# Kernel tuning notes

Measured on AMD Instinct MI355X. Metric: run time of the kernel, lower is better.

Reference implementation:

```python
import jax, jax.numpy as jnp
import numpy as np

D_MODEL = 1024
NUM_HEADS = 16
DEPTH = D_MODEL // NUM_HEADS
MAX_LEN = 5000


def _make_pe(d_model=D_MODEL, max_len=MAX_LEN):
    # Faithful to torch PositionalEncoding: pe shape [max_len, 1, d_model]
    position = np.arange(max_len, dtype=np.float32)[:, None]
    div_term = np.exp(np.arange(0, d_model, 2, dtype=np.float32) * (-np.log(10000.0) / d_model))
    pe = np.zeros((max_len, d_model), dtype=np.float32)
    pe[:, 0::2] = np.sin(position * div_term)
    pe[:, 1::2] = np.cos(position * div_term)
    return jnp.asarray(pe[:, None, :])  # [max_len, 1, d_model]


def setup_inputs() -> dict:
    key = jax.random.key(0)
    ks = jax.random.split(key, 11)
    B, S, D = 4, 2048, D_MODEL
    s = 1.0 / np.sqrt(D)
    inp = {
        "v": jax.random.normal(ks[0], (B, S, D), jnp.float32),
        "k": jax.random.normal(ks[1], (B, S, D), jnp.float32),
        "q": jax.random.normal(ks[2], (B, S, D), jnp.float32),
        "wq_w": jax.random.normal(ks[3], (D, D), jnp.float32) * s,
        "wq_b": jnp.zeros((D,), jnp.float32),
        "wk_w": jax.random.normal(ks[4], (D, D), jnp.float32) * s,
        "wk_b": jnp.zeros((D,), jnp.float32),
        "wv_w": jax.random.normal(ks[5], (D, D), jnp.float32) * s,
        "wv_b": jnp.zeros((D,), jnp.float32),
        "dense_w": jax.random.normal(ks[6], (D, D), jnp.float32) * s,
        "dense_b": jnp.zeros((D,), jnp.float32),
        "pe": _make_pe(),
    }
    return inp


def _split_heads(x, B):
    # [B, S, D] -> [B, H, S, depth]
    return x.reshape(B, -1, NUM_HEADS, DEPTH).transpose(0, 2, 1, 3)


def reference(v, k, q, wq_w, wq_b, wk_w, wk_b, wv_w, wv_b, dense_w, dense_b, pe):
    B = q.shape[0]
    # Faithful bug-reproduction: pe[:batch] has shape [B, 1, D], broadcast over seq.
    pe_b = pe[:B]  # [B, 1, D]
    q = q + pe_b
    k = k + pe_b
    v = v + pe_b
    # Linear layers (torch: x @ W.T + b)
    qh = _split_heads(q @ wq_w.T + wq_b, B)  # [B,H,Sq,d]
    kh = _split_heads(k @ wk_w.T + wk_b, B)  # [B,H,Sk,d]
    vh = _split_heads(v @ wv_w.T + wv_b, B)  # [B,H,Sk,d]
    scale = 1.0 / jnp.sqrt(jnp.float32(DEPTH))
    logits = jnp.einsum("bhqd,bhkd->bhqk", qh, kh) * scale
    attn = jax.nn.softmax(logits, axis=-1)
    out = jnp.einsum("bhqk,bhkd->bhqd", attn, vh)
    out = out.transpose(0, 2, 1, 3).reshape(B, -1, D_MODEL)
    return out @ dense_w.T + dense_b
```

## Files before the change

kernel.cpp:

```cpp
#include <hip/hip_runtime.h>
#include <hip/hip_bf16.h>

typedef short short8 __attribute__((ext_vector_type(8)));
typedef float f32x4 __attribute__((ext_vector_type(4)));
typedef float f32x16 __attribute__((ext_vector_type(16)));
typedef unsigned int uint4v __attribute__((ext_vector_type(4)));

#define MFMA16(a, b, c) __builtin_amdgcn_mfma_f32_16x16x32_bf16(a, b, c, 0, 0, 0)
#define MFMA32(a, b, c) __builtin_amdgcn_mfma_f32_32x32x16_bf16(a, b, c, 0, 0, 0)

typedef __attribute__((address_space(1))) const unsigned int gas_u32;
typedef __attribute__((address_space(3))) unsigned int las_u32;

__device__ inline void gll16(const void* g, void* l) {
    __builtin_amdgcn_global_load_lds((gas_u32*)g, (las_u32*)l, 16, 0, 0);
}

__device__ inline unsigned short f2bf(float f) {
    unsigned u = __builtin_bit_cast(unsigned, f);
    u += 0x7fff + ((u >> 16) & 1);
    return (unsigned short)(u >> 16);
}

__device__ inline unsigned pk_trunc(float a, float b) {
    unsigned ua = __builtin_bit_cast(unsigned, a);
    unsigned ub = __builtin_bit_cast(unsigned, b);
    return (ua >> 16) | (ub & 0xFFFF0000u);
}

__device__ inline float exp2_fast(float x) {
#if __has_builtin(__builtin_amdgcn_exp2f)
    return __builtin_amdgcn_exp2f(x);
#else
    float r; asm("v_exp_f32 %0, %1" : "=v"(r) : "v"(x)); return r;
#endif
}

__device__ inline void pl32_swap(unsigned &a, unsigned &b) {
    asm volatile("v_permlane32_swap_b32 %0, %1" : "+v"(a), "+v"(b));
}

__global__ void pe_cast3(const float* __restrict__ q, const float* __restrict__ k,
                         const float* __restrict__ v, const float* __restrict__ pe,
                         unsigned short* __restrict__ oq, unsigned short* __restrict__ ok,
                         unsigned short* __restrict__ ov) {
    const float* x = (blockIdx.y == 0) ? q : (blockIdx.y == 1) ? k : v;
    unsigned short* o = (blockIdx.y == 0) ? oq : (blockIdx.y == 1) ? ok : ov;
    int i = blockIdx.x * 256 + threadIdx.x;
    long e = (long)i * 4;
    int b = (int)(e >> 21);
    int d = (int)(e & 1023);
    float4 xv = reinterpret_cast<const float4*>(x)[i];
    float4 pv = *reinterpret_cast<const float4*>(pe + b * 1024 + d);
    ushort4 r;
    r.x = f2bf(xv.x + pv.x); r.y = f2bf(xv.y + pv.y);
    r.z = f2bf(xv.z + pv.z); r.w = f2bf(xv.w + pv.w);
    reinterpret_cast<ushort4*>(o)[i] = r;
}

__global__ void wcast4(const float* __restrict__ w0, const float* __restrict__ w1,
                       const float* __restrict__ w2, const float* __restrict__ w3,
                       unsigned short* __restrict__ o0) {
    const float* w = (blockIdx.y == 0) ? w0 : (blockIdx.y == 1) ? w1
                   : (blockIdx.y == 2) ? w2 : w3;
    unsigned short* o = o0 + (size_t)blockIdx.y * 1024 * 1024;
    int i = blockIdx.x * 256 + threadIdx.x;
    float4 xv = reinterpret_cast<const float4*>(w)[i];
    ushort4 r;
    r.x = f2bf(xv.x); r.y = f2bf(xv.y); r.z = f2bf(xv.z); r.w = f2bf(xv.w);
    reinterpret_cast<ushort4*>(o)[i] = r;
}

template <int MODE>
__global__ __launch_bounds__(256) void gemm_bt(const unsigned short* __restrict__ A,
                                               const unsigned short* __restrict__ W,
                                               const float* __restrict__ bias,
                                               void* __restrict__ out, float scale) {
    const int K = 1024;
    __shared__ unsigned short lsA[128 * 32];
    __shared__ unsigned short lsB[128 * 32];
    int tid = threadIdx.x;
    int wave = tid >> 6, lane = tid & 63, lg = lane >> 4, l15 = lane & 15;
    int brow = blockIdx.x * 128;
    int bcol = blockIdx.y * 128;
    int wr = wave >> 1, wc = wave & 1;

    f32x4 zero4 = {0.f, 0.f, 0.f, 0.f};
    f32x4 acc[4][4];
#pragma unroll
    for (int m = 0; m < 4; ++m)
#pragma unroll
        for (int n = 0; n < 4; ++n) acc[m][n] = zero4;

    for (int k0 = 0; k0 < K; k0 += 32) {
#pragma unroll
        for (int j = 0; j < 2; ++j) {
            int c = j * 256 + wave * 64 + lane;
            const unsigned short* srcA = A + ((long)(brow + (c >> 2)) * K + k0 + (c & 3) * 8);
            const unsigned short* srcB = W + ((long)(bcol + (c >> 2)) * K + k0 + (c & 3) * 8);
            char* dstA = (char*)lsA + (j * 256 + wave * 64) * 16;
            char* dstB = (char*)lsB + (j * 256 + wave * 64) * 16;
            gll16(srcA, dstA);
            gll16(srcB, dstB);
        }
        __syncthreads();
        short8 af[4], bf_[4];
#pragma unroll
        for (int m = 0; m < 4; ++m) {
            int row = wr * 64 + m * 16 + l15;
            af[m] = *(const short8*)((const char*)lsA + row * 64 + lg * 16);
        }
#pragma unroll
        for (int n = 0; n < 4; ++n) {
            int col = wc * 64 + n * 16 + l15;
            bf_[n] = *(const short8*)((const char*)lsB + col * 64 + lg * 16);
        }
#pragma unroll
        for (int m = 0; m < 4; ++m)
#pragma unroll
            for (int n = 0; n < 4; ++n) acc[m][n] = MFMA16(af[m], bf_[n], acc[m][n]);
        __syncthreads();
    }

#pragma unroll
    for (int m = 0; m < 4; ++m)
#pragma unroll
        for (int n = 0; n < 4; ++n) {
            int col = bcol + wc * 64 + n * 16 + l15;
            float bv = bias[col];
#pragma unroll
            for (int r = 0; r < 4; ++r) {
                int row = brow + wr * 64 + m * 16 + lg * 4 + r;
                float v = (acc[m][n][r] + bv) * scale;
                if (MODE == 0) {
                    int b = row >> 11, s = row & 2047, h = col >> 6, d = col & 63;
                    ((unsigned short*)out)[(((long)(b * 16 + h) * 2048 + s) * 64 + d)] = f2bf(v);
                } else if (MODE == 1) {
                    ((float*)out)[(long)row * 1024 + col] = v;
                } else {
                    int b = row >> 11, s = row & 2047;
                    ((unsigned short*)out)[((long)(b * 1024 + col)) * 2048 + s] = f2bf(v);
                }
            }
        }
}

__global__ __launch_bounds__(256) void attn_kernel(const unsigned short* __restrict__ Qh,
                                                   const unsigned short* __restrict__ Kh,
                                                   const unsigned short* __restrict__ Vt,
                                                   unsigned short* __restrict__ Om) {
    const int S = 2048;
    int flat = blockIdx.x;
    int nf_ = (flat & 7) * 128 + (flat >> 3);
    int qt = nf_ & 15;
    int bh = nf_ >> 4;
    int b = bh >> 4, h = bh & 15;

    int tid = threadIdx.x, wave = tid >> 6, lane = tid & 63;
    int l31 = lane & 31, hi = lane >> 5;

    __shared__ __align__(16) unsigned short Kl[2][4096];
    __shared__ __align__(16) unsigned short Vtl[2][4096];

    const unsigned short* Qb = Qh + (long)bh * S * 64;
    const unsigned short* Kb = Kh + (long)bh * S * 64;
    const unsigned short* Vb = Vt + (long)bh * 64 * S;

    int colS = ((((tid & 7) * 16) ^ (((tid >> 3) & 7) << 4)) >> 1);
    const unsigned short* srcK = Kb + (tid >> 3) * 64 + colS;
    const unsigned short* srcV = Vb + (tid >> 3) * 2048 + colS;

    short8 aq[4];
    {
        const unsigned short* qrow = Qb + (long)(qt * 128 + wave * 32 + l31) * 64 + hi * 8;
#pragma unroll
        for (int s = 0; s < 4; ++s) aq[s] = *(const short8*)(qrow + s * 16);
    }

    f32x16 oacc[2], lacc;
#pragma unroll
    for (int r = 0; r < 16; ++r) { oacc[0][r] = 0.f; oacc[1][r] = 0.f; lacc[r] = 0.f; }

    const short8 ones8 = {0x3F80, 0x3F80, 0x3F80, 0x3F80, 0x3F80, 0x3F80, 0x3F80, 0x3F80};

    int rb0 = l31 * 128;
    int swz = (l31 & 7) << 4;

#define STAGE(kt, bi) do {                                              \
        const unsigned short* sk = srcK + (kt) * 4096;                  \
        gll16(sk,         (char*)Kl[bi] + wave * 1024);                 \
        gll16(sk + 2048,  (char*)Kl[bi] + 4096 + wave * 1024);          \
        const unsigned short* sv = srcV + (kt) * 64;                    \
        gll16(sv,         (char*)Vtl[bi] + wave * 1024);                \
        gll16(sv + 65536, (char*)Vtl[bi] + 4096 + wave * 1024);         \
    } while (0)

    STAGE(0, 0);
    __syncthreads();

    for (int kt = 0; kt < S / 64; ++kt) {
        int cur = kt & 1;
        if (kt < S / 64 - 1) STAGE(kt + 1, cur ^ 1);

        const char* KlC = (const char*)Kl[cur];
        const char* VlC = (const char*)Vtl[cur];

        f32x16 sacc[2];
#pragma unroll
        for (int r = 0; r < 16; ++r) { sacc[0][r] = 0.f; sacc[1][r] = 0.f; }
#pragma unroll
        for (int blk = 0; blk < 2; ++blk)
#pragma unroll
            for (int s = 0; s < 4; ++s) {
                short8 kf = *(const short8*)(KlC + blk * 4096 + rb0 + ((32 * s + 16 * hi) ^ swz));
                sacc[blk] = MFMA32(kf, aq[s], sacc[blk]);
            }

#pragma unroll
        for (int blk = 0; blk < 2; ++blk)
#pragma unroll
            for (int r = 0; r < 16; ++r) sacc[blk][r] = exp2_fast(sacc[blk][r]);

#pragma unroll
        for (int s = 0; s < 4; ++s) {
            const int blk = s >> 1, base = (s & 1) * 8;
            unsigned q0 = pk_trunc(sacc[blk][base + 0], sacc[blk][base + 1]);
            unsigned q1 = pk_trunc(sacc[blk][base + 2], sacc[blk][base + 3]);
            unsigned q2 = pk_trunc(sacc[blk][base + 4], sacc[blk][base + 5]);
            unsigned q3 = pk_trunc(sacc[blk][base + 6], sacc[blk][base + 7]);
            pl32_swap(q0, q2);
            pl32_swap(q1, q3);
            uint4v pw; pw[0] = q0; pw[1] = q1; pw[2] = q2; pw[3] = q3;
            short8 pa = __builtin_bit_cast(short8, pw);
#pragma unroll
            for (int dblk = 0; dblk < 2; ++dblk) {
                short8 vf = *(const short8*)(VlC + dblk * 4096 + rb0 + ((32 * s + 16 * hi) ^ swz));
                oacc[dblk] = MFMA32(pa, vf, oacc[dblk]);
            }
            lacc = MFMA32(pa, ones8, lacc);
        }
        __syncthreads();
    }
#undef STAGE

    float inv[16];
#pragma unroll
    for (int r = 0; r < 16; ++r) inv[r] = 1.0f / lacc[r];

    int qrow0 = qt * 128 + wave * 32 + 4 * hi;
#pragma unroll
    for (int dblk = 0; dblk < 2; ++dblk)
#pragma unroll
        for (int r = 0; r < 16; ++r) {
            int qrow = qrow0 + (r & 3) + 8 * (r >> 2);
            int d = h * 64 + dblk * 32 + l31;
            float v = oacc[dblk][r] * inv[r];
            Om[((long)b * 2048 + qt * 0 + qrow) * 1024 + d] = f2bf(v);
        }
}

extern "C" void kernel_launch(void* const* d_in, const int* in_sizes, int n_in,
                              void* d_out, int out_size, void* d_ws, size_t ws_size,
                              hipStream_t stream) {
    const float* v_in = (const float*)d_in[0];
    const float* k_in = (const float*)d_in[1];
    const float* q_in = (const float*)d_in[2];
    const float* wq_w = (const float*)d_in[3];
    const float* wq_b = (const float*)d_in[4];
    const float* wk_w = (const float*)d_in[5];
    const float* wk_b = (const float*)d_in[6];
    const float* wv_w = (const float*)d_in[7];
    const float* wv_b = (const float*)d_in[8];
    const float* wd_w = (const float*)d_in[9];
    const float* wd_b = (const float*)d_in[10];
    const float* pe   = (const float*)d_in[11];

    const long SZ = 8192L * 1024 * 2;
    char* ws = (char*)d_ws;
    unsigned short* xq = (unsigned short*)(ws + 0);
    unsigned short* xk = (unsigned short*)(ws + SZ);
    unsigned short* xv = (unsigned short*)(ws + 2 * SZ);
    unsigned short* qh = (unsigned short*)(ws + 3 * SZ);
    unsigned short* kh = (unsigned short*)(ws + 4 * SZ);
    unsigned short* vt = (unsigned short*)(ws + 5 * SZ);
    unsigned short* wqb16 = (unsigned short*)(ws + 6 * SZ);
    unsigned short* wkb16 = wqb16 + 1024 * 1024;
    unsigned short* wvb16 = wkb16 + 1024 * 1024;
    unsigned short* wdb16 = wvb16 + 1024 * 1024;

    pe_cast3<<<dim3(8192, 3), 256, 0, stream>>>(q_in, k_in, v_in, pe, xq, xk, xv);
    wcast4<<<dim3(1024, 4), 256, 0, stream>>>(wq_w, wk_w, wv_w, wd_w, wqb16);

    const float QSCALE = 0.125f * 1.44269504088896f;
    dim3 gg(64, 8);
    gemm_bt<0><<<gg, 256, 0, stream>>>(xq, wqb16, wq_b, qh, QSCALE);
    gemm_bt<0><<<gg, 256, 0, stream>>>(xk, wkb16, wk_b, kh, 1.0f);
    gemm_bt<2><<<gg, 256, 0, stream>>>(xv, wvb16, wv_b, vt, 1.0f);
    unsigned short* om = xq;
    attn_kernel<<<1024, 256, 0, stream>>>(qh, kh, vt, om);
    gemm_bt<1><<<gg, 256, 0, stream>>>(om, wdb16, wd_b, d_out, 1.0f);
}
```

Measured before the change: 230.6 us.

## Merge QKV GEMMs into one launch and triple-buffer attention K/V loads

Replaces the three separate Q/K/V projection launches with a single 3D-grid launch whose z index selects input, weight, bias and output layout. The dense GEMM becomes its own specialised kernel. The attention kernel moves from double to triple buffering of the K/V tiles: it prefetches two tiles ahead, waits with explicit vmcnt counts and a raw barrier, and drops the trailing syncthreads. The goal is to cut launch gaps and tail effects and to hide more global-load latency, at the cost of more LDS per block and fragile hand-written wait counts.

Result: no change. 233.9 us (+1.4%).

```diff
diff --git a/kernel.cpp b/kernel.cpp
--- a/kernel.cpp
+++ b/kernel.cpp
@@ -71,11 +71,93 @@
     reinterpret_cast<ushort4*>(o)[i] = r;
 }
 
-template <int MODE>
-__global__ __launch_bounds__(256) void gemm_bt(const unsigned short* __restrict__ A,
-                                               const unsigned short* __restrict__ W,
-                                               const float* __restrict__ bias,
-                                               void* __restrict__ out, float scale) {
+__global__ __launch_bounds__(256) void gemm_qkv(const unsigned short* __restrict__ X0,
+                                                const unsigned short* __restrict__ W0,
+                                                const float* __restrict__ bq,
+                                                const float* __restrict__ bk,
+                                                const float* __restrict__ bv,
+                                                unsigned short* __restrict__ oq,
+                                                unsigned short* __restrict__ ok,
+                                                unsigned short* __restrict__ ov,
+                                                float qscale) {
+    const int K = 1024;
+    int z = blockIdx.z;
+    const unsigned short* A = X0 + (size_t)z * 8192 * 1024;
+    const unsigned short* W = W0 + (size_t)z * 1024 * 1024;
+    const float* bias = (z == 0) ? bq : (z == 1) ? bk : bv;
+    unsigned short* out = (z == 0) ? oq : (z == 1) ? ok : ov;
+    float scale = (z == 0) ? qscale : 1.0f;
+
+    __shared__ unsigned short lsA[128 * 32];
+    __shared__ unsigned short lsB[128 * 32];
+    int tid = threadIdx.x;
+    int wave = tid >> 6, lane = tid & 63, lg = lane >> 4, l15 = lane & 15;
+    int brow = blockIdx.x * 128;
+    int bcol = blockIdx.y * 128;
+    int wr = wave >> 1, wc = wave & 1;
+
+    f32x4 zero4 = {0.f, 0.f, 0.f, 0.f};
+    f32x4 acc[4][4];
+#pragma unroll
+    for (int m = 0; m < 4; ++m)
+#pragma unroll
+        for (int n = 0; n < 4; ++n) acc[m][n] = zero4;
+
+    for (int k0 = 0; k0 < K; k0 += 32) {
+#pragma unroll
+        for (int j = 0; j < 2; ++j) {
+            int c = j * 256 + wave * 64 + lane;
+            const unsigned short* srcA = A + ((long)(brow + (c >> 2)) * K + k0 + (c & 3) * 8);
+            const unsigned short* srcB = W + ((long)(bcol + (c >> 2)) * K + k0 + (c & 3) * 8);
+            char* dstA = (char*)lsA + (j * 256 + wave * 64) * 16;
+            char* dstB = (char*)lsB + (j * 256 + wave * 64) * 16;
+            gll16(srcA, dstA);
+            gll16(srcB, dstB);
+        }
+        __syncthreads();
+        short8 af[4], bf_[4];
+#pragma unroll
+        for (int m = 0; m < 4; ++m) {
+            int row = wr * 64 + m * 16 + l15;
+            af[m] = *(const short8*)((const char*)lsA + row * 64 + lg * 16);
+        }
+#pragma unroll
+        for (int n = 0; n < 4; ++n) {
+            int col = wc * 64 + n * 16 + l15;
+            bf_[n] = *(const short8*)((const char*)lsB + col * 64 + lg * 16);
+        }
+#pragma unroll
+        for (int m = 0; m < 4; ++m)
+#pragma unroll
+            for (int n = 0; n < 4; ++n) acc[m][n] = MFMA16(af[m], bf_[n], acc[m][n]);
+        __syncthreads();
+    }
+
+#pragma unroll
+    for (int m = 0; m < 4; ++m)
+#pragma unroll
+        for (int n = 0; n < 4; ++n) {
+            int col = bcol + wc * 64 + n * 16 + l15;
+            float bv_ = bias[col];
+#pragma unroll
+            for (int r = 0; r < 4; ++r) {
+                int row = brow + wr * 64 + m * 16 + lg * 4 + r;
+                float v = (acc[m][n][r] + bv_) * scale;
+                int b = row >> 11, s = row & 2047;
+                if (z < 2) {
+                    int h = col >> 6, d = col & 63;
+                    out[(((long)(b * 16 + h) * 2048 + s) * 64 + d)] = f2bf(v);
+                } else {
+                    out[((long)(b * 1024 + col)) * 2048 + s] = f2bf(v);
+                }
+            }
+        }
+}
+
+__global__ __launch_bounds__(256) void gemm_dense(const unsigned short* __restrict__ A,
+                                                  const unsigned short* __restrict__ W,
+                                                  const float* __restrict__ bias,
+                                                  float* __restrict__ out) {
     const int K = 1024;
     __shared__ unsigned short lsA[128 * 32];
     __shared__ unsigned short lsB[128 * 32];
@@ -131,16 +213,7 @@
 #pragma unroll
             for (int r = 0; r < 4; ++r) {
                 int row = brow + wr * 64 + m * 16 + lg * 4 + r;
-                float v = (acc[m][n][r] + bv) * scale;
-                if (MODE == 0) {
-                    int b = row >> 11, s = row & 2047, h = col >> 6, d = col & 63;
-                    ((unsigned short*)out)[(((long)(b * 16 + h) * 2048 + s) * 64 + d)] = f2bf(v);
-                } else if (MODE == 1) {
-                    ((float*)out)[(long)row * 1024 + col] = v;
-                } else {
-                    int b = row >> 11, s = row & 2047;
-                    ((unsigned short*)out)[((long)(b * 1024 + col)) * 2048 + s] = f2bf(v);
-                }
+                out[(long)row * 1024 + col] = acc[m][n][r] + bv;
             }
         }
 }
@@ -150,6 +223,7 @@
                                                    const unsigned short* __restrict__ Vt,
                                                    unsigned short* __restrict__ Om) {
     const int S = 2048;
+    const int NT = S / 64;
     int flat = blockIdx.x;
     int nf_ = (flat & 7) * 128 + (flat >> 3);
     int qt = nf_ & 15;
@@ -159,8 +233,8 @@
     int tid = threadIdx.x, wave = tid >> 6, lane = tid & 63;
     int l31 = lane & 31, hi = lane >> 5;
 
-    __shared__ __align__(16) unsigned short Kl[2][4096];
-    __shared__ __align__(16) unsigned short Vtl[2][4096];
+    __shared__ __align__(16) unsigned short Kl[3][4096];
+    __shared__ __align__(16) unsigned short Vtl[3][4096];
 
     const unsigned short* Qb = Qh + (long)bh * S * 64;
     const unsigned short* Kb = Kh + (long)bh * S * 64;
@@ -196,14 +270,17 @@
     } while (0)
 
     STAGE(0, 0);
-    __syncthreads();
-
-    for (int kt = 0; kt < S / 64; ++kt) {
-        int cur = kt & 1;
-        if (kt < S / 64 - 1) STAGE(kt + 1, cur ^ 1);
-
-        const char* KlC = (const char*)Kl[cur];
-        const char* VlC = (const char*)Vtl[cur];
+    STAGE(1, 1);
+
+    int bi = 0, sb = 2;
+    for (int kt = 0; kt < NT; ++kt) {
+        if (kt == NT - 1) { asm volatile("s_waitcnt vmcnt(0)" ::: "memory"); }
+        else              { asm volatile("s_waitcnt vmcnt(4)" ::: "memory"); }
+        __builtin_amdgcn_s_barrier();
+        if (kt < NT - 2) STAGE(kt + 2, sb);
+
+        const char* KlC = (const char*)Kl[bi];
+        const char* VlC = (const char*)Vtl[bi];
 
         f32x16 sacc[2];
 #pragma unroll
@@ -239,7 +316,8 @@
             }
             lacc = MFMA32(pa, ones8, lacc);
         }
-        __syncthreads();
+        bi = (bi == 2) ? 0 : bi + 1;
+        sb = (sb == 2) ? 0 : sb + 1;
     }
 #undef STAGE
 
@@ -255,7 +333,7 @@
             int qrow = qrow0 + (r & 3) + 8 * (r >> 2);
             int d = h * 64 + dblk * 32 + l31;
             float v = oacc[dblk][r] * inv[r];
-            Om[((long)b * 2048 + qt * 0 + qrow) * 1024 + d] = f2bf(v);
+            Om[((long)b * 2048 + qrow) * 1024 + d] = f2bf(v);
         }
 }
 
@@ -284,19 +362,15 @@
     unsigned short* kh = (unsigned short*)(ws + 4 * SZ);
     unsigned short* vt = (unsigned short*)(ws + 5 * SZ);
     unsigned short* wqb16 = (unsigned short*)(ws + 6 * SZ);
-    unsigned short* wkb16 = wqb16 + 1024 * 1024;
-    unsigned short* wvb16 = wkb16 + 1024 * 1024;
-    unsigned short* wdb16 = wvb16 + 1024 * 1024;
 
     pe_cast3<<<dim3(8192, 3), 256, 0, stream>>>(q_in, k_in, v_in, pe, xq, xk, xv);
     wcast4<<<dim3(1024, 4), 256, 0, stream>>>(wq_w, wk_w, wv_w, wd_w, wqb16);
 
     const float QSCALE = 0.125f * 1.44269504088896f;
-    dim3 gg(64, 8);
-    gemm_bt<0><<<gg, 256, 0, stream>>>(xq, wqb16, wq_b, qh, QSCALE);
-    gemm_bt<0><<<gg, 256, 0, stream>>>(xk, wkb16, wk_b, kh, 1.0f);
-    gemm_bt<2><<<gg, 256, 0, stream>>>(xv, wvb16, wv_b, vt, 1.0f);
+    gemm_qkv<<<dim3(64, 8, 3), 256, 0, stream>>>(xq, wqb16, wq_b, wk_b, wv_b,
+                                                 qh, kh, vt, QSCALE);
     unsigned short* om = xq;
     attn_kernel<<<1024, 256, 0, stream>>>(qh, kh, vt, om);
-    gemm_bt<1><<<gg, 256, 0, stream>>>(om, wdb16, wd_b, d_out, 1.0f);
-}
+    gemm_dense<<<dim3(64, 8), 256, 0, stream>>>(om, wqb16 + 3L * 1024 * 1024, wd_b,
+                                                (float*)d_out);
+}
```
